# Optimization experiments

Measured on AMD Instinct MI355X. Metric: run time of the kernel, lower is better.

Reference implementation:

```python
import jax, jax.numpy as jnp
import numpy as np
from jax import lax

D_MODEL = 64
D_STATE = 128
D_INNER = 128  # d_model * expand_factor; must equal D_STATE for the original code to broadcast
BATCH = 4
SEQ = 1024
LN_EPS = 1e-5


def setup_inputs() -> dict:
    key = jax.random.key(0)
    ks = jax.random.split(key, 12)
    s = 0.05
    return {
        "x": jax.random.normal(ks[0], (BATCH, SEQ, D_MODEL), jnp.float32),
        "W_in": jax.random.normal(ks[1], (2 * D_INNER, D_MODEL), jnp.float32) * s,
        "W_delta": jax.random.normal(ks[2], (D_INNER, D_MODEL), jnp.float32) * s,
        "b_delta": jax.random.normal(ks[3], (D_INNER,), jnp.float32) * s,
        "W_B": jax.random.normal(ks[4], (D_STATE, D_MODEL), jnp.float32) * s,
        "b_B": jax.random.normal(ks[5], (D_STATE,), jnp.float32) * s,
        "W_C": jax.random.normal(ks[6], (D_STATE, D_MODEL), jnp.float32) * s,
        "b_C": jax.random.normal(ks[7], (D_STATE,), jnp.float32) * s,
        "A": jax.random.normal(ks[8], (D_INNER, D_STATE), jnp.float32) * 0.01,
        "W_out": jax.random.normal(ks[9], (D_MODEL, D_INNER), jnp.float32) * s,
        "ln_w": jnp.ones((D_MODEL,), jnp.float32),
        "ln_b": jnp.zeros((D_MODEL,), jnp.float32),
    }


def _layer_norm(x, w, b):
    mu = x.mean(-1, keepdims=True)
    var = ((x - mu) ** 2).mean(-1, keepdims=True)
    return (x - mu) * lax.rsqrt(var + LN_EPS) * w + b


def reference(x, W_in, W_delta, b_delta, W_B, b_B, W_C, b_C, A, W_out, ln_w, ln_b):
    # projections
    xp = jnp.einsum('bld,ed->ble', x, W_in)            # (B, L, 2*d_inner)
    x_ssm, gate = xp[..., :D_INNER], xp[..., D_INNER:]
    delta = jax.nn.softplus(jnp.einsum('bld,id->bli', x, W_delta) + b_delta)  # (B, L, d_inner)
    Bm = jnp.einsum('bld,sd->bls', x, W_B) + b_B        # (B, L, d_state)
    Cm = jnp.einsum('bld,sd->bls', x, W_C) + b_C        # (B, L, d_state)

    # A_discrete.mean(dim=1): mean over d_inner of exp(delta * A)
    Abar = jnp.exp(delta[..., :, None] * A).mean(axis=2)  # (B, L, d_state)
    x_pool = x_ssm.mean(axis=-1)                          # (B, L) mean over d_inner
    Bx = Bm * x_pool[..., None]                           # (B, L, d_state)

    def step(h, inp):
        a_t, bx_t, c_t = inp                              # each (B, d_state)
        h = a_t * h + bx_t
        y = (c_t * h).sum(axis=-1)                        # (B,)
        return h, y

    h0 = jnp.zeros((x.shape[0], D_STATE), x.dtype)
    _, ys = lax.scan(step, h0,
                     (jnp.swapaxes(Abar, 0, 1), jnp.swapaxes(Bx, 0, 1), jnp.swapaxes(Cm, 0, 1)))
    y = jnp.swapaxes(ys, 0, 1)[..., None]                 # (B, L, 1) -> broadcast over d_inner

    y = y * jax.nn.silu(gate)                             # (B, L, d_inner)
    out = jnp.einsum('bli,di->bld', y, W_out)             # (B, L, d_model)
    return _layer_norm(out + x, ln_w, ln_b)
```

## Files before the change

### kernel.cpp

```cpp
#include <hip/hip_runtime.h>
#include <math.h>

#define NB   4
#define SL   1024
#define NTOK (NB*SL)
#define DM   64
#define DI   128
#define DSt  128
#define SEGLEN 8
#define NSEG (SL/SEGLEN)
#define NSEG_ALL (NB*NSEG)

#define OFF_GATE   0
#define OFF_DELTA  (OFF_GATE  + NTOK*DI)
#define OFF_BM     (OFF_DELTA + NTOK*DI)
#define OFF_CM     (OFF_BM    + NTOK*DSt)
#define OFF_XPOOL  (OFF_CM    + NTOK*DSt)
#define OFF_ABAR   (OFF_XPOOL + NTOK)
#define OFF_HEND   (OFF_ABAR  + NTOK*DSt)
#define OFF_P      (OFF_HEND  + NSEG_ALL*DSt)
#define OFF_W4     (OFF_P     + NSEG_ALL*DSt)

#define PROJ_TOK 16
#define PROJ_TG  (NTOK/PROJ_TOK)

static __device__ __forceinline__ float wave64_sum(float v) {
#pragma unroll
    for (int m = 32; m >= 1; m >>= 1) v += __shfl_xor(v, m, 64);
    return v;
}

static __device__ __forceinline__ float fast_exp2(float x) {
    float r;
    asm("v_exp_f32 %0, %1" : "=v"(r) : "v"(x));
    return r;
}

static __device__ __forceinline__ float softplus_f(float x) {
    return fmaxf(x, 0.f) + __logf(1.f + __expf(-fabsf(x)));
}

static __device__ __forceinline__ void pin4(float4& v) {
    asm volatile("" : "+v"(v.x), "+v"(v.y), "+v"(v.z), "+v"(v.w));
}

__global__ __launch_bounds__(256, 2) void k_proj(
    const float* __restrict__ x, const float* __restrict__ W_in,
    const float* __restrict__ W_delta, const float* __restrict__ b_delta,
    const float* __restrict__ W_B, const float* __restrict__ b_B,
    const float* __restrict__ W_C, const float* __restrict__ b_C,
    const float* __restrict__ W_out, float* __restrict__ ws)
{
    __shared__ float  xl[PROJ_TOK*DM];
    __shared__ float4 Wl[DI*16];
    const int tid = threadIdx.x;

    if (blockIdx.x == 4*PROJ_TG) {
        const float4* Wg = (const float4*)W_out;
        float4* W4 = (float4*)(ws + OFF_W4);
#pragma unroll
        for (int j = 0; j < 8; ++j) {
            const int f = tid + j*256;
            const int d = f >> 5, q = f & 31;
            W4[q*64 + d] = Wg[f];
        }
        return;
    }

    const int l   = tid & 63;
    const int w   = tid >> 6;
    const int cat = blockIdx.x >> 8;
    const int tg  = blockIdx.x & 255;
    const int tok0 = tg * PROJ_TOK;

    const float* Wbase; const float* bias; float* dst;
    if      (cat == 0) { Wbase = W_in + DI*DM; bias = nullptr; dst = ws + OFF_GATE;  }
    else if (cat == 1) { Wbase = W_delta;      bias = b_delta; dst = ws + OFF_DELTA; }
    else if (cat == 2) { Wbase = W_B;          bias = b_B;     dst = ws + OFF_BM;    }
    else               { Wbase = W_C;          bias = b_C;     dst = ws + OFF_CM;    }

    {
        const float4* xg = (const float4*)(x + tok0*DM);
        ((float4*)xl)[tid] = xg[tid];
        const float4* Wg = (const float4*)Wbase;
#pragma unroll
        for (int j = 0; j < 8; ++j) {
            const int f = tid + j*256;
            const int row = f >> 4, k = f & 15;
            Wl[row*16 + (k ^ (row & 15))] = Wg[f];
        }
    }
    __syncthreads();

    float4 w0[16], w1[16];
#pragma unroll
    for (int k = 0; k < 16; ++k) {
        w0[k] = Wl[l*16      + (k ^ (l & 15))];
        w1[k] = Wl[(l+64)*16 + (k ^ (l & 15))];
    }
#pragma unroll
    for (int k = 0; k < 16; ++k) { pin4(w0[k]); pin4(w1[k]); }

    float bias0 = 0.f, bias1 = 0.f;
    if (bias) { bias0 = bias[l]; bias1 = bias[l+64]; }

#pragma unroll
    for (int it = 0; it < PROJ_TOK/4; ++it) {
        const int tl = it*4 + w;
        float a0=0.f,a1=0.f,a2=0.f,a3=0.f, c0=0.f,c1=0.f,c2=0.f,c3=0.f;
#pragma unroll
        for (int k = 0; k < 16; ++k) {
            const float4 xv = *(const float4*)(xl + tl*DM + 4*k);
            a0 = fmaf(w0[k].x, xv.x, a0);
            a1 = fmaf(w0[k].y, xv.y, a1);
            a2 = fmaf(w0[k].z, xv.z, a2);
            a3 = fmaf(w0[k].w, xv.w, a3);
            c0 = fmaf(w1[k].x, xv.x, c0);
            c1 = fmaf(w1[k].y, xv.y, c1);
            c2 = fmaf(w1[k].z, xv.z, c2);
            c3 = fmaf(w1[k].w, xv.w, c3);
        }
        float ra = (a0+a1) + (a2+a3) + bias0;
        float rb = (c0+c1) + (c2+c3) + bias1;
        if (cat == 1) { ra = softplus_f(ra); rb = softplus_f(rb); }
        const int tok = tok0 + tl;
        dst[tok*128 + l]      = ra;
        dst[tok*128 + 64 + l] = rb;
    }

    if (cat == 0) {
        float wp = 0.f;
#pragma unroll 8
        for (int i = 0; i < DI; ++i) wp += W_in[i*DM + l];
        wp *= (1.0f/DI);
#pragma unroll
        for (int it = 0; it < PROJ_TOK/4; ++it) {
            const int tl = it*4 + w;
            float v = xl[tl*DM + l] * wp;
            v = wave64_sum(v);
            if (l == 0) ws[OFF_XPOOL + tok0 + tl] = v;
        }
    }
}

__global__ __launch_bounds__(256) void k_abar_scan1(const float* __restrict__ A,
                                                    float* __restrict__ ws)
{
    __shared__ float psum[4][SEGLEN][64];
    __shared__ float abL[SEGLEN][64];
    const int tid  = threadIdx.x;
    const int lane = tid & 63;
    const int igrp = tid >> 6;
    const int g    = blockIdx.x >> 1;
    const int sh   = blockIdx.x & 1;
    const int s    = sh*64 + lane;
    const int t0   = g * SEGLEN;

    float areg[32];
#pragma unroll
    for (int i = 0; i < 32; ++i)
        areg[i] = A[(igrp*32 + i)*DSt + s] * 1.44269504f;

    const float* delta = ws + OFF_DELTA;
    float*       Abar  = ws + OFF_ABAR;

#pragma unroll
    for (int t = 0; t < SEGLEN; ++t) {
        const float* dv = delta + (t0 + t)*DI + igrp*32;
        float a0=0.f,a1=0.f,a2=0.f,a3=0.f;
#pragma unroll
        for (int q = 0; q < 8; ++q) {
            const float4 d4 = *(const float4*)(dv + 4*q);
            a0 += fast_exp2(d4.x * areg[4*q    ]);
            a1 += fast_exp2(d4.y * areg[4*q + 1]);
            a2 += fast_exp2(d4.z * areg[4*q + 2]);
            a3 += fast_exp2(d4.w * areg[4*q + 3]);
        }
        psum[igrp][t][lane] = (a0+a1) + (a2+a3);
    }
    __syncthreads();

#pragma unroll
    for (int it = tid; it < SEGLEN*64; it += 256) {
        const int t = it >> 6, l2 = it & 63;
        float v = (psum[0][t][l2] + psum[1][t][l2])
                + (psum[2][t][l2] + psum[3][t][l2]);
        v *= (1.0f/DI);
        abL[t][l2] = v;
        Abar[(t0 + t)*DSt + sh*64 + l2] = v;
    }
    __syncthreads();

    if (tid < 64) {
        const float* Bm    = ws + OFF_BM;
        const float* xpool = ws + OFF_XPOOL;
        float bx[SEGLEN];
#pragma unroll
        for (int t = 0; t < SEGLEN; ++t)
            bx[t] = Bm[(t0 + t)*DSt + s] * xpool[t0 + t];
        float h = 0.f, pr = 1.f;
#pragma unroll
        for (int t = 0; t < SEGLEN; ++t) {
            const float a = abL[t][lane];
            h = fmaf(a, h, bx[t]);
            pr *= a;
        }
        ws[OFF_HEND + g*DSt + s] = h;
        ws[OFF_P    + g*DSt + s] = pr;
    }
}

__global__ __launch_bounds__(128) void k_tail(
    const float* __restrict__ x, const float* __restrict__ ln_w,
    const float* __restrict__ ln_b, const float* __restrict__ ws,
    float* __restrict__ out)
{
    __shared__ float prod[SEGLEN][132];
    __shared__ float y_lds[SEGLEN];
    __shared__ float vbuf[2][DI];

    const int tid = threadIdx.x;
    const int s   = tid;
    const int b   = blockIdx.x >> 7;
    const int seg = blockIdx.x & 127;
    const int t0  = b*SL + seg*SEGLEN;

    const float* Abar  = ws + OFF_ABAR;
    const float* Bm    = ws + OFF_BM;
    const float* Cm    = ws + OFF_CM;
    const float* xpool = ws + OFF_XPOOL;
    const float* hend  = ws + OFF_HEND;
    const float* P     = ws + OFF_P;

    float aA[SEGLEN], aB[SEGLEN], aC[SEGLEN];
#pragma unroll
    for (int t = 0; t < SEGLEN; ++t) {
        aA[t] = Abar[(t0 + t)*DSt + s];
        aB[t] = Bm[(t0 + t)*DSt + s] * xpool[t0 + t];
        aC[t] = Cm[(t0 + t)*DSt + s];
    }
    float h = 0.f;
#pragma unroll 8
    for (int j = 0; j < seg; ++j) {
        const int idx = (b*NSEG + j)*DSt + s;
        h = fmaf(P[idx], h, hend[idx]);
    }
#pragma unroll
    for (int t = 0; t < SEGLEN; ++t) {
        h = fmaf(aA[t], h, aB[t]);
        prod[t][s] = aC[t] * h;
    }
    __syncthreads();

    {
        const int t = s >> 4, r = s & 15;
        float4 u0 = *(const float4*)(&prod[t][r*8]);
        float4 u1 = *(const float4*)(&prod[t][r*8 + 4]);
        float acc = ((u0.x+u0.y) + (u0.z+u0.w)) + ((u1.x+u1.y) + (u1.z+u1.w));
#pragma unroll
        for (int m = 1; m <= 8; m <<= 1) acc += __shfl_xor(acc, m, 64);
        if (r == 0) y_lds[t] = acc;
    }
    __syncthreads();

    const float* gate = ws + OFF_GATE;
    const float4* W4  = (const float4*)(ws + OFF_W4);
    const int d  = tid & 63;
    const int wv = tid >> 6;
    const float lw = ln_w[d], lb = ln_b[d];
#pragma unroll 2
    for (int jt = 0; jt < 4; ++jt) {
        const int tl  = wv*4 + jt;
        const int tok = t0 + tl;
        const float yt = y_lds[tl];
        const float g0 = gate[tok*DI + d];
        const float g1 = gate[tok*DI + 64 + d];
        vbuf[wv][d]      = yt * (g0 / (1.f + __expf(-g0)));
        vbuf[wv][64 + d] = yt * (g1 / (1.f + __expf(-g1)));

        float ac0 = 0.f, ac1 = 0.f, ac2 = 0.f, ac3 = 0.f;
#pragma unroll 8
        for (int q = 0; q < 32; ++q) {
            const float4 wv4 = W4[q*64 + d];
            const float4 vv  = *(const float4*)(&vbuf[wv][q*4]);
            ac0 = fmaf(wv4.x, vv.x, ac0);
            ac1 = fmaf(wv4.y, vv.y, ac1);
            ac2 = fmaf(wv4.z, vv.z, ac2);
            ac3 = fmaf(wv4.w, vv.w, ac3);
        }
        const float z  = (ac0+ac1) + (ac2+ac3) + x[tok*DM + d];
        const float s1 = wave64_sum(z);
        const float s2 = wave64_sum(z*z);
        const float mu  = s1 * (1.f/64.f);
        const float var = s2 * (1.f/64.f) - mu*mu;
        out[tok*DM + d] = (z - mu) * rsqrtf(var + 1e-5f) * lw + lb;
    }
}

extern "C" void kernel_launch(void* const* d_in, const int* in_sizes, int n_in,
                              void* d_out, int out_size, void* d_ws, size_t ws_size,
                              hipStream_t stream) {
    const float* x       = (const float*)d_in[0];
    const float* W_in    = (const float*)d_in[1];
    const float* W_delta = (const float*)d_in[2];
    const float* b_delta = (const float*)d_in[3];
    const float* W_B     = (const float*)d_in[4];
    const float* b_B     = (const float*)d_in[5];
    const float* W_C     = (const float*)d_in[6];
    const float* b_C     = (const float*)d_in[7];
    const float* A       = (const float*)d_in[8];
    const float* W_out   = (const float*)d_in[9];
    const float* ln_w    = (const float*)d_in[10];
    const float* ln_b    = (const float*)d_in[11];
    float* out = (float*)d_out;
    float* ws  = (float*)d_ws;

    hipLaunchKernelGGL(k_proj, dim3(4*PROJ_TG + 1), dim3(256), 0, stream,
                       x, W_in, W_delta, b_delta, W_B, b_B, W_C, b_C, W_out, ws);
    hipLaunchKernelGGL(k_abar_scan1, dim3(2*NSEG_ALL), dim3(256), 0, stream, A, ws);
    hipLaunchKernelGGL(k_tail,       dim3(NSEG_ALL),   dim3(128), 0, stream,
                       x, ln_w, ln_b, ws, out);
}
```

Measured before the change: 51.52 us.

## Fuse three-kernel pipeline into one cooperative kernel with grid syncs

Replaces the three separate launches (projection, Abar/segment scan, tail) with one cooperative kernel of 512 blocks that uses grid.sync between phases. Each block handles two projection units, then one segment's Abar and local scan, then the cross-segment combine, output projection and layer norm. Abar values stay in shared memory across phases. The aim is to remove launch gaps and inter-kernel drain. In exchange it pays for grid-wide barriers and gets less parallelism in the projection phase. The original launches remain as a fallback if the cooperative launch fails.

```diff
diff --git a/kernel.cpp b/kernel.cpp
--- a/kernel.cpp
+++ b/kernel.cpp
@@ -1,5 +1,8 @@
 #include <hip/hip_runtime.h>
+#include <hip/hip_cooperative_groups.h>
 #include <math.h>
+
+namespace cg = cooperative_groups;
 
 #define NB   4
 #define SL   1024
@@ -42,6 +45,261 @@
 
 static __device__ __forceinline__ void pin4(float4& v) {
     asm volatile("" : "+v"(v.x), "+v"(v.y), "+v"(v.z), "+v"(v.w));
+}
+
+__global__ __launch_bounds__(256, 2) void k_fused(
+    const float* __restrict__ x, const float* __restrict__ W_in,
+    const float* __restrict__ W_delta, const float* __restrict__ b_delta,
+    const float* __restrict__ W_B, const float* __restrict__ b_B,
+    const float* __restrict__ W_C, const float* __restrict__ b_C,
+    const float* __restrict__ A, const float* __restrict__ W_out,
+    const float* __restrict__ ln_w, const float* __restrict__ ln_b,
+    float* __restrict__ ws, float* __restrict__ out)
+{
+    __shared__ __align__(16) unsigned char smem[40960];
+    float4* Wl   = (float4*)smem;
+    float*  xl   = (float*)(smem + 32768);
+    float*  psum = (float*)smem;
+    float*  prod = (float*)smem;
+    float*  vbuf = (float*)(smem + 8192);
+    float*  yb   = (float*)(smem + 10240);
+    float*  abC  = (float*)(smem + 36864);
+
+    const int tid = threadIdx.x;
+    cg::grid_group grid = cg::this_grid();
+
+    if (blockIdx.x < 8) {
+        const int f = blockIdx.x*256 + tid;
+        const int dd = f >> 5, q = f & 31;
+        ((float4*)(ws + OFF_W4))[q*64 + dd] = ((const float4*)W_out)[f];
+    }
+
+#pragma unroll 1
+    for (int u = 0; u < 2; ++u) {
+        const int unit = blockIdx.x*2 + u;
+        const int cat  = unit >> 8;
+        const int tg   = unit & 255;
+        const int tok0 = tg * PROJ_TOK;
+        const int l    = tid & 63;
+        const int w    = tid >> 6;
+
+        const float* Wbase; const float* bias; float* dst;
+        if      (cat == 0) { Wbase = W_in + DI*DM; bias = nullptr; dst = ws + OFF_GATE;  }
+        else if (cat == 1) { Wbase = W_delta;      bias = b_delta; dst = ws + OFF_DELTA; }
+        else if (cat == 2) { Wbase = W_B;          bias = b_B;     dst = ws + OFF_BM;    }
+        else               { Wbase = W_C;          bias = b_C;     dst = ws + OFF_CM;    }
+
+        __syncthreads();
+        {
+            const float4* xg = (const float4*)(x + tok0*DM);
+            ((float4*)xl)[tid] = xg[tid];
+            const float4* Wg = (const float4*)Wbase;
+#pragma unroll
+            for (int j = 0; j < 8; ++j) {
+                const int f = tid + j*256;
+                const int row = f >> 4, k = f & 15;
+                Wl[row*16 + (k ^ (row & 15))] = Wg[f];
+            }
+        }
+        __syncthreads();
+
+        float4 w0[16], w1[16];
+#pragma unroll
+        for (int k = 0; k < 16; ++k) {
+            w0[k] = Wl[l*16      + (k ^ (l & 15))];
+            w1[k] = Wl[(l+64)*16 + (k ^ (l & 15))];
+        }
+#pragma unroll
+        for (int k = 0; k < 16; ++k) { pin4(w0[k]); pin4(w1[k]); }
+
+        float bias0 = 0.f, bias1 = 0.f;
+        if (bias) { bias0 = bias[l]; bias1 = bias[l+64]; }
+
+#pragma unroll
+        for (int it = 0; it < PROJ_TOK/4; ++it) {
+            const int tl = it*4 + w;
+            float a0=0.f,a1=0.f,a2=0.f,a3=0.f, c0=0.f,c1=0.f,c2=0.f,c3=0.f;
+#pragma unroll
+            for (int k = 0; k < 16; ++k) {
+                const float4 xv = *(const float4*)(xl + tl*DM + 4*k);
+                a0 = fmaf(w0[k].x, xv.x, a0);
+                a1 = fmaf(w0[k].y, xv.y, a1);
+                a2 = fmaf(w0[k].z, xv.z, a2);
+                a3 = fmaf(w0[k].w, xv.w, a3);
+                c0 = fmaf(w1[k].x, xv.x, c0);
+                c1 = fmaf(w1[k].y, xv.y, c1);
+                c2 = fmaf(w1[k].z, xv.z, c2);
+                c3 = fmaf(w1[k].w, xv.w, c3);
+            }
+            float ra = (a0+a1) + (a2+a3) + bias0;
+            float rb = (c0+c1) + (c2+c3) + bias1;
+            if (cat == 1) { ra = softplus_f(ra); rb = softplus_f(rb); }
+            const int tok = tok0 + tl;
+            dst[tok*128 + l]      = ra;
+            dst[tok*128 + 64 + l] = rb;
+        }
+
+        if (cat == 0) {
+            float wp = 0.f;
+#pragma unroll 8
+            for (int i = 0; i < DI; ++i) wp += W_in[i*DM + l];
+            wp *= (1.0f/DI);
+#pragma unroll
+            for (int it = 0; it < PROJ_TOK/4; ++it) {
+                const int tl = it*4 + w;
+                float v = xl[tl*DM + l] * wp;
+                v = wave64_sum(v);
+                if (l == 0) ws[OFF_XPOOL + tok0 + tl] = v;
+            }
+        }
+    }
+
+    grid.sync();
+
+    {
+        const int g  = blockIdx.x;
+        const int t0 = g * SEGLEN;
+        const int lane = tid & 63;
+        const int igrp = tid >> 6;
+        const float* delta = ws + OFF_DELTA;
+
+#pragma unroll 1
+        for (int u = 0; u < 2; ++u) {
+            const int sh = u;
+            const int s  = sh*64 + lane;
+
+            float areg[32];
+#pragma unroll
+            for (int i = 0; i < 32; ++i)
+                areg[i] = A[(igrp*32 + i)*DSt + s] * 1.44269504f;
+
+            __syncthreads();
+#pragma unroll
+            for (int t = 0; t < SEGLEN; ++t) {
+                const float* dv = delta + (t0 + t)*DI + igrp*32;
+                float a0=0.f,a1=0.f,a2=0.f,a3=0.f;
+#pragma unroll
+                for (int q = 0; q < 8; ++q) {
+                    const float4 d4 = *(const float4*)(dv + 4*q);
+                    a0 += fast_exp2(d4.x * areg[4*q    ]);
+                    a1 += fast_exp2(d4.y * areg[4*q + 1]);
+                    a2 += fast_exp2(d4.z * areg[4*q + 2]);
+                    a3 += fast_exp2(d4.w * areg[4*q + 3]);
+                }
+                psum[(igrp*SEGLEN + t)*64 + lane] = (a0+a1) + (a2+a3);
+            }
+            __syncthreads();
+
+#pragma unroll
+            for (int it = tid; it < SEGLEN*64; it += 256) {
+                const int t = it >> 6, l2 = it & 63;
+                float v = (psum[(0*SEGLEN + t)*64 + l2] + psum[(1*SEGLEN + t)*64 + l2])
+                        + (psum[(2*SEGLEN + t)*64 + l2] + psum[(3*SEGLEN + t)*64 + l2]);
+                abC[t*DSt + sh*64 + l2] = v * (1.0f/DI);
+            }
+            __syncthreads();
+
+            if (tid < 64) {
+                const float* Bm    = ws + OFF_BM;
+                const float* xpool = ws + OFF_XPOOL;
+                float bx[SEGLEN];
+#pragma unroll
+                for (int t = 0; t < SEGLEN; ++t)
+                    bx[t] = Bm[(t0 + t)*DSt + s] * xpool[t0 + t];
+                float h = 0.f, pr = 1.f;
+#pragma unroll
+                for (int t = 0; t < SEGLEN; ++t) {
+                    const float a = abC[t*DSt + s];
+                    h = fmaf(a, h, bx[t]);
+                    pr *= a;
+                }
+                ws[OFF_HEND + g*DSt + s] = h;
+                ws[OFF_P    + g*DSt + s] = pr;
+            }
+        }
+    }
+
+    grid.sync();
+
+    {
+        const int b   = blockIdx.x >> 7;
+        const int seg = blockIdx.x & 127;
+        const int t0  = b*SL + seg*SEGLEN;
+
+        __syncthreads();
+        if (tid < 128) {
+            const int s = tid;
+            const float* Bm    = ws + OFF_BM;
+            const float* Cm    = ws + OFF_CM;
+            const float* xpool = ws + OFF_XPOOL;
+            const float* hend  = ws + OFF_HEND;
+            const float* P     = ws + OFF_P;
+
+            float aA[SEGLEN], aB[SEGLEN], aC[SEGLEN];
+#pragma unroll
+            for (int t = 0; t < SEGLEN; ++t) {
+                aA[t] = abC[t*DSt + s];
+                aB[t] = Bm[(t0 + t)*DSt + s] * xpool[t0 + t];
+                aC[t] = Cm[(t0 + t)*DSt + s];
+            }
+            float h = 0.f;
+#pragma unroll 8
+            for (int j = 0; j < seg; ++j) {
+                const int idx = (b*NSEG + j)*DSt + s;
+                h = fmaf(P[idx], h, hend[idx]);
+            }
+#pragma unroll
+            for (int t = 0; t < SEGLEN; ++t) {
+                h = fmaf(aA[t], h, aB[t]);
+                prod[t*132 + s] = aC[t] * h;
+            }
+        }
+        __syncthreads();
+
+        if (tid < 128) {
+            const int t = tid >> 4, r = tid & 15;
+            float4 u0 = *(const float4*)(&prod[t*132 + r*8]);
+            float4 u1 = *(const float4*)(&prod[t*132 + r*8 + 4]);
+            float acc = ((u0.x+u0.y) + (u0.z+u0.w)) + ((u1.x+u1.y) + (u1.z+u1.w));
+#pragma unroll
+            for (int m = 1; m <= 8; m <<= 1) acc += __shfl_xor(acc, m, 64);
+            if (r == 0) yb[t] = acc;
+        }
+        __syncthreads();
+
+        const float* gate = ws + OFF_GATE;
+        const float4* W4  = (const float4*)(ws + OFF_W4);
+        const int d  = tid & 63;
+        const int wv = tid >> 6;
+        const float lw = ln_w[d], lb = ln_b[d];
+#pragma unroll
+        for (int jt = 0; jt < 2; ++jt) {
+            const int tl  = wv*2 + jt;
+            const int tok = t0 + tl;
+            const float yt = yb[tl];
+            const float g0 = gate[tok*DI + d];
+            const float g1 = gate[tok*DI + 64 + d];
+            vbuf[wv*DI + d]      = yt * (g0 / (1.f + __expf(-g0)));
+            vbuf[wv*DI + 64 + d] = yt * (g1 / (1.f + __expf(-g1)));
+
+            float ac0 = 0.f, ac1 = 0.f, ac2 = 0.f, ac3 = 0.f;
+#pragma unroll 8
+            for (int q = 0; q < 32; ++q) {
+                const float4 wv4 = W4[q*64 + d];
+                const float4 vv  = *(const float4*)(&vbuf[wv*DI + q*4]);
+                ac0 = fmaf(wv4.x, vv.x, ac0);
+                ac1 = fmaf(wv4.y, vv.y, ac1);
+                ac2 = fmaf(wv4.z, vv.z, ac2);
+                ac3 = fmaf(wv4.w, vv.w, ac3);
+            }
+            const float z  = (ac0+ac1) + (ac2+ac3) + x[tok*DM + d];
+            const float s1 = wave64_sum(z);
+            const float s2 = wave64_sum(z*z);
+            const float mu  = s1 * (1.f/64.f);
+            const float var = s2 * (1.f/64.f) - mu*mu;
+            out[tok*DM + d] = (z - mu) * rsqrtf(var + 1e-5f) * lw + lb;
+        }
+    }
 }
 
 __global__ __launch_bounds__(256, 2) void k_proj(
@@ -315,9 +573,20 @@
     float* out = (float*)d_out;
     float* ws  = (float*)d_ws;
 
-    hipLaunchKernelGGL(k_proj, dim3(4*PROJ_TG + 1), dim3(256), 0, stream,
-                       x, W_in, W_delta, b_delta, W_B, b_B, W_C, b_C, W_out, ws);
-    hipLaunchKernelGGL(k_abar_scan1, dim3(2*NSEG_ALL), dim3(256), 0, stream, A, ws);
-    hipLaunchKernelGGL(k_tail,       dim3(NSEG_ALL),   dim3(128), 0, stream,
-                       x, ln_w, ln_b, ws, out);
-}
+    void* args[] = {
+        (void*)&x, (void*)&W_in, (void*)&W_delta, (void*)&b_delta,
+        (void*)&W_B, (void*)&b_B, (void*)&W_C, (void*)&b_C,
+        (void*)&A, (void*)&W_out, (void*)&ln_w, (void*)&ln_b,
+        (void*)&ws, (void*)&out
+    };
+    hipError_t err = hipLaunchCooperativeKernel((const void*)k_fused,
+                                                dim3(NSEG_ALL), dim3(256),
+                                                args, 0, stream);
+    if (err != hipSuccess) {
+        hipLaunchKernelGGL(k_proj, dim3(4*PROJ_TG + 1), dim3(256), 0, stream,
+                           x, W_in, W_delta, b_delta, W_B, b_B, W_C, b_C, W_out, ws);
+        hipLaunchKernelGGL(k_abar_scan1, dim3(2*NSEG_ALL), dim3(256), 0, stream, A, ws);
+        hipLaunchKernelGGL(k_tail,       dim3(NSEG_ALL),   dim3(128), 0, stream,
+                           x, ln_w, ln_b, ws, out);
+    }
+}
```

New measurement: 166.8 us. 224% more time.
